# Performance work log

Measured on AMD Instinct MI355X. Metric: run time of the kernel, lower is better.

## Reference

```python
import jax
import jax.numpy as jnp
import numpy as np

L, H_DIM = 8192, 128
ATTN_WINDOW, STRIDE = 3, 2


def setup_inputs() -> dict:
    key = jax.random.key(0)
    k1, k2, k3, k4, k5 = jax.random.split(key, 5)
    input_sequence = jax.random.normal(k1, (L, H_DIM), dtype=jnp.float32)
    # zoh-discretized diagonal decays exp(Lambda*Delta) lie in (0,1)
    Lambda_bar = jax.random.uniform(k2, (H_DIM, H_DIM), dtype=jnp.float32,
                                    minval=0.5, maxval=0.999)
    C_tilde = jax.random.normal(k3, (H_DIM, H_DIM), dtype=jnp.float32) / jnp.sqrt(
        jnp.float32(H_DIM))
    w_q = jax.random.normal(k4, (ATTN_WINDOW, ATTN_WINDOW), dtype=jnp.float32) * 0.1
    D = jax.random.normal(k5, (ATTN_WINDOW,), dtype=jnp.float32)
    return {
        "input_sequence": input_sequence,
        "Lambda_bar": Lambda_bar,
        "C_tilde": C_tilde,
        "w_q": w_q,
        "D": D,
        "attn_window": ATTN_WINDOW,
        "stride": STRIDE,
    }


def reference(input_sequence, Lambda_bar, C_tilde, w_q, D, attn_window, stride):
    # input_sequence: (L, H); Lambda_bar, C_tilde: (H, H); w_q: (W, W); D: (W,)
    Lseq, H = input_sequence.shape
    num_windows = (Lseq - attn_window) // stride + 1
    idx = jnp.arange(num_windows)[:, None] * stride + jnp.arange(attn_window)
    windows = input_sequence[idx]  # (T, W, H)

    # local self-attention per window: x.T @ w_q @ x  -> (T, H, H), axes (t, a, d)
    lsa = jnp.einsum("twa,wv,tvd->tad", windows, w_q, windows)

    # diagonal linear SSM scan over windows, vectorized over both H axes:
    # carry[a, d] = Lambda_bar[a, d] * carry[a, d] + lsa[t, a, d]
    def step(carry, inp):
        carry = Lambda_bar * carry + inp
        return carry, carry

    init = jnp.zeros((H, H), dtype=input_sequence.dtype)
    _, zs = jax.lax.scan(step, init, lsa)  # (T, a, d)

    # original stacks per-d scans on axis=1 giving (T, d, a), then C_tilde @ u
    # contracts d: out[t, h, a] = sum_d C_tilde[h, d] * zs[t, a, d]
    zs_out = jnp.einsum("hd,tad->tha", C_tilde, zs)  # (T, H, H)

    # os = vmap(u.T @ D): (T, H)
    os = jnp.einsum("twh,w->th", windows, D)
    return zs_out, os
```

## Files before the change

### kernel.cpp

```cpp
#include <hip/hip_runtime.h>

#define L_   8192
#define H_   128
#define T_   4095
#define CH_  16
#define NC_  256

typedef __bf16 bf16x8 __attribute__((ext_vector_type(8)));
typedef unsigned short ushort8 __attribute__((ext_vector_type(8)));
typedef float f32x4 __attribute__((ext_vector_type(4)));

__device__ __forceinline__ unsigned short f2bf(float f) {
    unsigned int u = __builtin_bit_cast(unsigned int, f);
    u += 0x7fffu + ((u >> 16) & 1u);
    return (unsigned short)(u >> 16);
}

__global__ __launch_bounds__(256) void os_kernel(const float* __restrict__ X,
                                                 const float* __restrict__ Dv,
                                                 float* __restrict__ os) {
    int i = blockIdx.x * 256 + threadIdx.x;
    if (i >= T_ * H_) return;
    int t = i >> 7, h = i & 127;
    const float* xr = X + (size_t)(2 * t) * H_ + h;
    os[i] = Dv[0] * xr[0] + Dv[1] * xr[H_] + Dv[2] * xr[2 * H_];
}

__global__ __launch_bounds__(256) void pass1_kernel(const float* __restrict__ X,
                                                    const float* __restrict__ Lam,
                                                    const float* __restrict__ wq,
                                                    float* __restrict__ ebuf) {
    const int c     = blockIdx.x;
    const int entry = blockIdx.y * 256 + threadIdx.x;
    const int a = entry >> 7, d = entry & 127;
    const float lam = Lam[entry];
    const float w00 = wq[0], w01 = wq[1], w02 = wq[2];
    const float w10 = wq[3], w11 = wq[4], w12 = wq[5];
    const float w20 = wq[6], w21 = wq[7], w22 = wq[8];

    const int t0 = c * CH_;
    const int t1 = min(t0 + CH_, T_);
    const float* xr0 = X + (size_t)(2 * t0) * H_;
    float xa0 = xr0[a], xa1 = xr0[H_ + a];
    float xd0 = xr0[d], xd1 = xr0[H_ + d];
    float z = 0.f;
    for (int t = t0; t < t1; ++t) {
        const float* x2 = X + (size_t)(2 * t) * H_ + 2 * H_;
        float xa2 = x2[a], xd2 = x2[d];
        float y0 = w00 * xd0 + w01 * xd1 + w02 * xd2;
        float y1 = w10 * xd0 + w11 * xd1 + w12 * xd2;
        float y2 = w20 * xd0 + w21 * xd1 + w22 * xd2;
        float u  = xa0 * y0 + xa1 * y1 + xa2 * y2;
        z = fmaf(lam, z, u);
        xa0 = xa2; xd0 = xd2;
        xa1 = x2[H_ + a]; xd1 = x2[H_ + d];
    }
    ebuf[(size_t)c * (H_ * H_) + entry] = z;
}

__global__ __launch_bounds__(256) void pass2_kernel(const float* __restrict__ Lam,
                                                    float* __restrict__ ebuf) {
    const int entry = blockIdx.x * 256 + threadIdx.x;
    const float lam = Lam[entry];
    float p = lam * lam; p = p * p; p = p * p; p = p * p;
    float z = 0.f;
    for (int cb = 0; cb < NC_; cb += 8) {
        float tmp[8];
        #pragma unroll
        for (int i = 0; i < 8; ++i)
            tmp[i] = ebuf[(size_t)(cb + i) * (H_ * H_) + entry];
        #pragma unroll
        for (int i = 0; i < 8; ++i) {
            ebuf[(size_t)(cb + i) * (H_ * H_) + entry] = z;
            z = fmaf(p, z, tmp[i]);
        }
    }
}

__global__ __launch_bounds__(256) void pass3_kernel(const float* __restrict__ X,
                                                    const float* __restrict__ Lam,
                                                    const float* __restrict__ Cm,
                                                    const float* __restrict__ wq,
                                                    const float* __restrict__ carry,
                                                    float* __restrict__ out) {
    __shared__ unsigned short z_s[32][136];
    __shared__ float y_s[3][128];
    __shared__ float xa_s[3][32];

    const int tid  = threadIdx.x;
    const int c    = blockIdx.x;
    const int a0   = blockIdx.y * 32;
    const int lane = tid & 63;
    const int wave = tid >> 6;
    const int m    = lane & 15;
    const int q    = lane >> 4;

    ushort8 afrag[2][4];
    #pragma unroll
    for (int mi = 0; mi < 2; ++mi) {
        const int h = (wave * 2 + mi) * 16 + m;
        #pragma unroll
        for (int kt = 0; kt < 4; ++kt) {
            const float* src = Cm + h * 128 + kt * 32 + q * 8;
            ushort8 v;
            #pragma unroll
            for (int j = 0; j < 8; ++j) v[j] = f2bf(src[j]);
            afrag[mi][kt] = v;
        }
    }

    const int a_l = tid & 31;
    const int dg  = tid >> 5;
    float z[16], lam[16];
    {
        const float* lp = Lam   + (size_t)(a0 + a_l) * 128 + dg * 16;
        const float* cp = carry + (size_t)c * (H_ * H_) + (size_t)(a0 + a_l) * 128 + dg * 16;
        #pragma unroll
        for (int j = 0; j < 16; ++j) { lam[j] = lp[j]; z[j] = cp[j]; }
    }
    const float w00 = wq[0], w01 = wq[1], w02 = wq[2];
    const float w10 = wq[3], w11 = wq[4], w12 = wq[5];
    const float w20 = wq[6], w21 = wq[7], w22 = wq[8];

    const int t0 = c * CH_;
    const int t1 = min(t0 + CH_, T_);

    for (int t = t0; t < t1; ++t) {
        __syncthreads();
        const float* xr = X + (size_t)(2 * t) * H_;
        if (tid < 128) {
            float xd0 = xr[tid], xd1 = xr[H_ + tid], xd2 = xr[2 * H_ + tid];
            y_s[0][tid] = w00 * xd0 + w01 * xd1 + w02 * xd2;
            y_s[1][tid] = w10 * xd0 + w11 * xd1 + w12 * xd2;
            y_s[2][tid] = w20 * xd0 + w21 * xd1 + w22 * xd2;
        } else if (tid < 224) {
            int li = tid - 128;
            xa_s[li >> 5][li & 31] = xr[(li >> 5) * H_ + a0 + (li & 31)];
        }
        __syncthreads();

        {
            const float xa0 = xa_s[0][a_l], xa1 = xa_s[1][a_l], xa2 = xa_s[2][a_l];
            #pragma unroll
            for (int j = 0; j < 16; ++j) {
                const int d = dg * 16 + j;
                float u = xa0 * y_s[0][d] + xa1 * y_s[1][d] + xa2 * y_s[2][d];
                z[j] = fmaf(lam[j], z[j], u);
            }
            ushort8 zb0, zb1;
            #pragma unroll
            for (int j = 0; j < 8; ++j) { zb0[j] = f2bf(z[j]); zb1[j] = f2bf(z[j + 8]); }
            *(ushort8*)&z_s[a_l][dg * 16]     = zb0;
            *(ushort8*)&z_s[a_l][dg * 16 + 8] = zb1;
        }
        __syncthreads();

        f32x4 acc[2][2] = {};
        #pragma unroll
        for (int kt = 0; kt < 4; ++kt) {
            bf16x8 b0 = __builtin_bit_cast(bf16x8, *(const ushort8*)&z_s[m][kt * 32 + q * 8]);
            bf16x8 b1 = __builtin_bit_cast(bf16x8, *(const ushort8*)&z_s[16 + m][kt * 32 + q * 8]);
            #pragma unroll
            for (int mi = 0; mi < 2; ++mi) {
                bf16x8 a = __builtin_bit_cast(bf16x8, afrag[mi][kt]);
                acc[mi][0] = __builtin_amdgcn_mfma_f32_16x16x32_bf16(a, b0, acc[mi][0], 0, 0, 0);
                acc[mi][1] = __builtin_amdgcn_mfma_f32_16x16x32_bf16(a, b1, acc[mi][1], 0, 0, 0);
            }
        }
        float* ob = out + (size_t)t * (H_ * H_) + a0;
        #pragma unroll
        for (int mi = 0; mi < 2; ++mi) {
            const int hb = (wave * 2 + mi) * 16 + q * 4;
            #pragma unroll
            for (int r = 0; r < 4; ++r) {
                ob[(size_t)(hb + r) * H_ + m]      = acc[mi][0][r];
                ob[(size_t)(hb + r) * H_ + 16 + m] = acc[mi][1][r];
            }
        }
    }
}

extern "C" void kernel_launch(void* const* d_in, const int* in_sizes, int n_in,
                              void* d_out, int out_size, void* d_ws, size_t ws_size,
                              hipStream_t stream) {
    const float* X   = (const float*)d_in[0];
    const float* Lam = (const float*)d_in[1];
    const float* Cm  = (const float*)d_in[2];
    const float* wq  = (const float*)d_in[3];
    const float* Dv  = (const float*)d_in[4];
    float* out = (float*)d_out;
    float* ebuf = (float*)d_ws;

    os_kernel<<<(T_ * H_ + 255) / 256, 256, 0, stream>>>(X, Dv, out + (size_t)T_ * H_ * H_);
    pass1_kernel<<<dim3(NC_, 64), 256, 0, stream>>>(X, Lam, wq, ebuf);
    pass2_kernel<<<64, 256, 0, stream>>>(Lam, ebuf);
    pass3_kernel<<<dim3(NC_, 4), 256, 0, stream>>>(X, Lam, Cm, wq, ebuf, out);
}
```

Baseline: 361.3 us.

## Fuse os into pass3, restructure pass1 with shared y, swap MFMA operands for vector stores

The separate os kernel is folded into pass3, where the block with blockIdx.y==0 computes os from the X rows it already loads. pass1 is rebuilt to share the w_q-projected y vectors through LDS, with each thread keeping 16 accumulators, matching pass3's tiling and launching far fewer blocks. In pass3 the MFMA operands are swapped so each lane holds four consecutive output columns, which allows 16-byte vector stores instead of scalar strided stores. Trade-offs: pass1 now has fewer blocks and adds per-step syncs, and the os work lands on only one quarter of the pass3 blocks.

```diff
diff --git a/kernel.cpp b/kernel.cpp
--- a/kernel.cpp
+++ b/kernel.cpp
@@ -16,107 +16,24 @@
     return (unsigned short)(u >> 16);
 }
 
-__global__ __launch_bounds__(256) void os_kernel(const float* __restrict__ X,
-                                                 const float* __restrict__ Dv,
-                                                 float* __restrict__ os) {
-    int i = blockIdx.x * 256 + threadIdx.x;
-    if (i >= T_ * H_) return;
-    int t = i >> 7, h = i & 127;
-    const float* xr = X + (size_t)(2 * t) * H_ + h;
-    os[i] = Dv[0] * xr[0] + Dv[1] * xr[H_] + Dv[2] * xr[2 * H_];
-}
-
 __global__ __launch_bounds__(256) void pass1_kernel(const float* __restrict__ X,
                                                     const float* __restrict__ Lam,
                                                     const float* __restrict__ wq,
                                                     float* __restrict__ ebuf) {
-    const int c     = blockIdx.x;
-    const int entry = blockIdx.y * 256 + threadIdx.x;
-    const int a = entry >> 7, d = entry & 127;
-    const float lam = Lam[entry];
-    const float w00 = wq[0], w01 = wq[1], w02 = wq[2];
-    const float w10 = wq[3], w11 = wq[4], w12 = wq[5];
-    const float w20 = wq[6], w21 = wq[7], w22 = wq[8];
-
-    const int t0 = c * CH_;
-    const int t1 = min(t0 + CH_, T_);
-    const float* xr0 = X + (size_t)(2 * t0) * H_;
-    float xa0 = xr0[a], xa1 = xr0[H_ + a];
-    float xd0 = xr0[d], xd1 = xr0[H_ + d];
-    float z = 0.f;
-    for (int t = t0; t < t1; ++t) {
-        const float* x2 = X + (size_t)(2 * t) * H_ + 2 * H_;
-        float xa2 = x2[a], xd2 = x2[d];
-        float y0 = w00 * xd0 + w01 * xd1 + w02 * xd2;
-        float y1 = w10 * xd0 + w11 * xd1 + w12 * xd2;
-        float y2 = w20 * xd0 + w21 * xd1 + w22 * xd2;
-        float u  = xa0 * y0 + xa1 * y1 + xa2 * y2;
-        z = fmaf(lam, z, u);
-        xa0 = xa2; xd0 = xd2;
-        xa1 = x2[H_ + a]; xd1 = x2[H_ + d];
-    }
-    ebuf[(size_t)c * (H_ * H_) + entry] = z;
-}
-
-__global__ __launch_bounds__(256) void pass2_kernel(const float* __restrict__ Lam,
-                                                    float* __restrict__ ebuf) {
-    const int entry = blockIdx.x * 256 + threadIdx.x;
-    const float lam = Lam[entry];
-    float p = lam * lam; p = p * p; p = p * p; p = p * p;
-    float z = 0.f;
-    for (int cb = 0; cb < NC_; cb += 8) {
-        float tmp[8];
-        #pragma unroll
-        for (int i = 0; i < 8; ++i)
-            tmp[i] = ebuf[(size_t)(cb + i) * (H_ * H_) + entry];
-        #pragma unroll
-        for (int i = 0; i < 8; ++i) {
-            ebuf[(size_t)(cb + i) * (H_ * H_) + entry] = z;
-            z = fmaf(p, z, tmp[i]);
-        }
-    }
-}
-
-__global__ __launch_bounds__(256) void pass3_kernel(const float* __restrict__ X,
-                                                    const float* __restrict__ Lam,
-                                                    const float* __restrict__ Cm,
-                                                    const float* __restrict__ wq,
-                                                    const float* __restrict__ carry,
-                                                    float* __restrict__ out) {
-    __shared__ unsigned short z_s[32][136];
     __shared__ float y_s[3][128];
     __shared__ float xa_s[3][32];
 
-    const int tid  = threadIdx.x;
-    const int c    = blockIdx.x;
-    const int a0   = blockIdx.y * 32;
-    const int lane = tid & 63;
-    const int wave = tid >> 6;
-    const int m    = lane & 15;
-    const int q    = lane >> 4;
-
-    ushort8 afrag[2][4];
-    #pragma unroll
-    for (int mi = 0; mi < 2; ++mi) {
-        const int h = (wave * 2 + mi) * 16 + m;
-        #pragma unroll
-        for (int kt = 0; kt < 4; ++kt) {
-            const float* src = Cm + h * 128 + kt * 32 + q * 8;
-            ushort8 v;
-            #pragma unroll
-            for (int j = 0; j < 8; ++j) v[j] = f2bf(src[j]);
-            afrag[mi][kt] = v;
-        }
-    }
-
+    const int tid = threadIdx.x;
+    const int c   = blockIdx.x;
+    const int a0  = blockIdx.y * 32;
     const int a_l = tid & 31;
     const int dg  = tid >> 5;
+
     float z[16], lam[16];
     {
-        const float* lp = Lam   + (size_t)(a0 + a_l) * 128 + dg * 16;
-        const float* cp = carry + (size_t)c * (H_ * H_) + (size_t)(a0 + a_l) * 128 + dg * 16;
-        #pragma unroll
-        for (int j = 0; j < 16; ++j) { lam[j] = lp[j]; z[j] = cp[j]; }
+        const float* lp = Lam + (size_t)(a0 + a_l) * H_ + dg * 16;
+        #pragma unroll
+        for (int j = 0; j < 16; ++j) { lam[j] = lp[j]; z[j] = 0.f; }
     }
     const float w00 = wq[0], w01 = wq[1], w02 = wq[2];
     const float w10 = wq[3], w11 = wq[4], w12 = wq[5];
@@ -138,6 +55,104 @@
             xa_s[li >> 5][li & 31] = xr[(li >> 5) * H_ + a0 + (li & 31)];
         }
         __syncthreads();
+        const float xa0 = xa_s[0][a_l], xa1 = xa_s[1][a_l], xa2 = xa_s[2][a_l];
+        #pragma unroll
+        for (int j = 0; j < 16; ++j) {
+            const int d = dg * 16 + j;
+            float u = xa0 * y_s[0][d] + xa1 * y_s[1][d] + xa2 * y_s[2][d];
+            z[j] = fmaf(lam[j], z[j], u);
+        }
+    }
+    float* ep = ebuf + (size_t)c * (H_ * H_) + (size_t)(a0 + a_l) * H_ + dg * 16;
+    #pragma unroll
+    for (int j = 0; j < 16; ++j) ep[j] = z[j];
+}
+
+__global__ __launch_bounds__(256) void pass2_kernel(const float* __restrict__ Lam,
+                                                    float* __restrict__ ebuf) {
+    const int entry = blockIdx.x * 256 + threadIdx.x;
+    const float lam = Lam[entry];
+    float p = lam * lam; p = p * p; p = p * p; p = p * p;
+    float z = 0.f;
+    for (int cb = 0; cb < NC_; cb += 8) {
+        float tmp[8];
+        #pragma unroll
+        for (int i = 0; i < 8; ++i)
+            tmp[i] = ebuf[(size_t)(cb + i) * (H_ * H_) + entry];
+        #pragma unroll
+        for (int i = 0; i < 8; ++i) {
+            ebuf[(size_t)(cb + i) * (H_ * H_) + entry] = z;
+            z = fmaf(p, z, tmp[i]);
+        }
+    }
+}
+
+__global__ __launch_bounds__(256) void pass3_kernel(const float* __restrict__ X,
+                                                    const float* __restrict__ Lam,
+                                                    const float* __restrict__ Cm,
+                                                    const float* __restrict__ wq,
+                                                    const float* __restrict__ Dv,
+                                                    const float* __restrict__ carry,
+                                                    float* __restrict__ out,
+                                                    float* __restrict__ os) {
+    __shared__ unsigned short z_s[32][136];
+    __shared__ float y_s[3][128];
+    __shared__ float xa_s[3][32];
+
+    const int tid  = threadIdx.x;
+    const int c    = blockIdx.x;
+    const int a0   = blockIdx.y * 32;
+    const int lane = tid & 63;
+    const int wave = tid >> 6;
+    const int m    = lane & 15;
+    const int q    = lane >> 4;
+
+    ushort8 cfrag[2][4];
+    #pragma unroll
+    for (int ni = 0; ni < 2; ++ni) {
+        const int h = (wave * 2 + ni) * 16 + m;
+        #pragma unroll
+        for (int kt = 0; kt < 4; ++kt) {
+            const float* src = Cm + h * H_ + kt * 32 + q * 8;
+            ushort8 v;
+            #pragma unroll
+            for (int j = 0; j < 8; ++j) v[j] = f2bf(src[j]);
+            cfrag[ni][kt] = v;
+        }
+    }
+
+    const int a_l = tid & 31;
+    const int dg  = tid >> 5;
+    float z[16], lam[16];
+    {
+        const float* lp = Lam   + (size_t)(a0 + a_l) * H_ + dg * 16;
+        const float* cp = carry + (size_t)c * (H_ * H_) + (size_t)(a0 + a_l) * H_ + dg * 16;
+        #pragma unroll
+        for (int j = 0; j < 16; ++j) { lam[j] = lp[j]; z[j] = cp[j]; }
+    }
+    const float w00 = wq[0], w01 = wq[1], w02 = wq[2];
+    const float w10 = wq[3], w11 = wq[4], w12 = wq[5];
+    const float w20 = wq[6], w21 = wq[7], w22 = wq[8];
+    const float d0 = Dv[0], d1 = Dv[1], d2 = Dv[2];
+    const bool do_os = (blockIdx.y == 0);
+
+    const int t0 = c * CH_;
+    const int t1 = min(t0 + CH_, T_);
+
+    for (int t = t0; t < t1; ++t) {
+        __syncthreads();
+        const float* xr = X + (size_t)(2 * t) * H_;
+        if (tid < 128) {
+            float xd0 = xr[tid], xd1 = xr[H_ + tid], xd2 = xr[2 * H_ + tid];
+            y_s[0][tid] = w00 * xd0 + w01 * xd1 + w02 * xd2;
+            y_s[1][tid] = w10 * xd0 + w11 * xd1 + w12 * xd2;
+            y_s[2][tid] = w20 * xd0 + w21 * xd1 + w22 * xd2;
+            if (do_os) os[t * H_ + tid] = d0 * xd0 + d1 * xd1 + d2 * xd2;
+        } else if (tid < 224) {
+            int li = tid - 128;
+            xa_s[li >> 5][li & 31] = xr[(li >> 5) * H_ + a0 + (li & 31)];
+        }
+        __syncthreads();
 
         {
             const float xa0 = xa_s[0][a_l], xa1 = xa_s[1][a_l], xa2 = xa_s[2][a_l];
@@ -158,23 +173,22 @@
         f32x4 acc[2][2] = {};
         #pragma unroll
         for (int kt = 0; kt < 4; ++kt) {
-            bf16x8 b0 = __builtin_bit_cast(bf16x8, *(const ushort8*)&z_s[m][kt * 32 + q * 8]);
-            bf16x8 b1 = __builtin_bit_cast(bf16x8, *(const ushort8*)&z_s[16 + m][kt * 32 + q * 8]);
-            #pragma unroll
-            for (int mi = 0; mi < 2; ++mi) {
-                bf16x8 a = __builtin_bit_cast(bf16x8, afrag[mi][kt]);
-                acc[mi][0] = __builtin_amdgcn_mfma_f32_16x16x32_bf16(a, b0, acc[mi][0], 0, 0, 0);
-                acc[mi][1] = __builtin_amdgcn_mfma_f32_16x16x32_bf16(a, b1, acc[mi][1], 0, 0, 0);
+            bf16x8 za = __builtin_bit_cast(bf16x8, *(const ushort8*)&z_s[m][kt * 32 + q * 8]);
+            bf16x8 zb = __builtin_bit_cast(bf16x8, *(const ushort8*)&z_s[16 + m][kt * 32 + q * 8]);
+            #pragma unroll
+            for (int ni = 0; ni < 2; ++ni) {
+                bf16x8 cf = __builtin_bit_cast(bf16x8, cfrag[ni][kt]);
+                acc[0][ni] = __builtin_amdgcn_mfma_f32_16x16x32_bf16(za, cf, acc[0][ni], 0, 0, 0);
+                acc[1][ni] = __builtin_amdgcn_mfma_f32_16x16x32_bf16(zb, cf, acc[1][ni], 0, 0, 0);
             }
         }
         float* ob = out + (size_t)t * (H_ * H_) + a0;
         #pragma unroll
         for (int mi = 0; mi < 2; ++mi) {
-            const int hb = (wave * 2 + mi) * 16 + q * 4;
-            #pragma unroll
-            for (int r = 0; r < 4; ++r) {
-                ob[(size_t)(hb + r) * H_ + m]      = acc[mi][0][r];
-                ob[(size_t)(hb + r) * H_ + 16 + m] = acc[mi][1][r];
+            #pragma unroll
+            for (int ni = 0; ni < 2; ++ni) {
+                const int h = (wave * 2 + ni) * 16 + m;
+                *(f32x4*)&ob[(size_t)h * H_ + mi * 16 + q * 4] = acc[mi][ni];
             }
         }
     }
@@ -189,10 +203,10 @@
     const float* wq  = (const float*)d_in[3];
     const float* Dv  = (const float*)d_in[4];
     float* out = (float*)d_out;
+    float* os  = out + (size_t)T_ * H_ * H_;
     float* ebuf = (float*)d_ws;
 
-    os_kernel<<<(T_ * H_ + 255) / 256, 256, 0, stream>>>(X, Dv, out + (size_t)T_ * H_ * H_);
-    pass1_kernel<<<dim3(NC_, 64), 256, 0, stream>>>(X, Lam, wq, ebuf);
+    pass1_kernel<<<dim3(NC_, 4), 256, 0, stream>>>(X, Lam, wq, ebuf);
     pass2_kernel<<<64, 256, 0, stream>>>(Lam, ebuf);
-    pass3_kernel<<<dim3(NC_, 4), 256, 0, stream>>>(X, Lam, Cm, wq, ebuf, out);
-}
+    pass3_kernel<<<dim3(NC_, 4), 256, 0, stream>>>(X, Lam, Cm, wq, Dv, ebuf, out, os);
+}
```

Result: faster. 346.3 us (-4.2%).
